# Kernel optimization log

Measured on AMD Instinct MI355X. Metric: run time of the kernel, lower is better.

## Reference

```python
import jax, jax.numpy as jnp
import numpy as np

N = 100000   # nodes
E = 1600000  # edges
G = 64       # graphs
D = 64       # latent_dim
NF = 128     # num_node_feats
EF = 32      # num_edge_feats
NV = 5000    # num_node_val_feats
LV = 3       # max_lv
EPS = 1e-5


def setup_inputs() -> dict:
    key = jax.random.key(0)
    ks = jax.random.split(key, 16)
    s = 0.05
    return {
        "node_feat": jax.random.normal(ks[0], (N, NF), jnp.float32),
        "edge_feat": jax.random.normal(ks[1], (E, EF), jnp.float32),
        "w_n2l_W": jax.random.normal(ks[2], (NF, D), jnp.float32) * s,
        "w_n2l_b": jnp.zeros((D,), jnp.float32),
        "node_val_embedding": jax.random.normal(ks[3], (NV, D), jnp.float32) * s,
        "w_e2l_W": jax.random.normal(ks[4], (LV + 1, EF, D), jnp.float32) * s,
        "w_e2l_b": jnp.zeros((LV + 1, D), jnp.float32),
        "conv_W": jax.random.normal(ks[5], (LV, D, D), jnp.float32) * s,
        "conv_b": jnp.zeros((LV, D), jnp.float32),
        "l2_W": jax.random.normal(ks[6], (LV, D, D), jnp.float32) * s,
        "l2_b": jnp.zeros((LV, D), jnp.float32),
        "msg_g": jnp.ones((LV + 1, D), jnp.float32),
        "msg_b": jnp.zeros((LV + 1, D), jnp.float32),
        "hid_g": jnp.ones((LV, D), jnp.float32),
        "hid_b": jnp.zeros((LV, D), jnp.float32),
        "out_W": jax.random.normal(ks[7], (D, D), jnp.float32) * s,
        "out_b": jnp.zeros((D,), jnp.float32),
        "edge_from": jax.random.randint(ks[8], (E,), 0, N, jnp.int32),
        "edge_to": jax.random.randint(ks[9], (E,), 0, N, jnp.int32),
        "g_idx": jnp.sort(jax.random.randint(ks[10], (N,), 0, G, jnp.int32)),
        "node_val_idx": jax.random.randint(ks[11], (N,), 0, NV, jnp.int32),
    }


def _bn(x, g, b):
    # BatchNorm1d in training mode: biased batch stats
    m = jnp.mean(x, axis=0)
    v = jnp.mean(jnp.square(x - m), axis=0)
    return (x - m) * jax.lax.rsqrt(v + EPS) * g + b


def reference(node_feat, edge_feat, w_n2l_W, w_n2l_b, node_val_embedding,
              w_e2l_W, w_e2l_b, conv_W, conv_b, l2_W, l2_b,
              msg_g, msg_b, hid_g, hid_b, out_W, out_b,
              edge_from, edge_to, g_idx, node_val_idx):
    act = jax.nn.relu
    # input node transform + sparse node-value embedding (one-hot spmm == gather)
    h = node_feat @ w_n2l_W + w_n2l_b + node_val_embedding[node_val_idx]
    # edge->node pool for level 0
    e0 = edge_feat @ w_e2l_W[0] + w_e2l_b[0]
    h = h + jax.ops.segment_sum(e0, edge_to, num_segments=N)
    h = _bn(act(h), msg_g[0], msg_b[0])
    for lv in range(LV):
        # MessagePassing with add-aggr: gather sources, scatter-add to targets, then Linear
        agg = jax.ops.segment_sum(h[edge_from], edge_to, num_segments=N)
        node_linear = agg @ conv_W[lv] + conv_b[lv]
        e = edge_feat @ w_e2l_W[lv + 1] + w_e2l_b[lv + 1]
        merged = act(node_linear + jax.ops.segment_sum(e, edge_to, num_segments=N))
        merged = _bn(merged, hid_g[lv], hid_b[lv])
        h = _bn(act(merged @ l2_W[lv] + l2_b[lv] + h), msg_g[lv + 1], msg_b[lv + 1])
    # readout: gnn_out='last', readout_agg='max', act_last=True, bn=False
    pooled = jax.ops.segment_max(h, g_idx, num_segments=G)
    return act(pooled @ out_W + out_b)
```

## Files before the change

kernel.cpp:

```cpp
#include <hip/hip_runtime.h>
#include <math.h>

#define NN 100000
#define EE 1600000
#define GG 64
#define DD 64
#define NF 128
#define EF 32
#define LVL 3
#define EPSBN 1e-5f
#define NTILES ((NN + 63) / 64)
#define NBKT 391

typedef unsigned short u16;
typedef unsigned int u32;
typedef unsigned long long u64;
typedef short s4v __attribute__((ext_vector_type(4)));
typedef short bf16x8 __attribute__((ext_vector_type(8)));
typedef float f32x4 __attribute__((ext_vector_type(4)));

__device__ __forceinline__ float4 ld4(const float* p) { return *(const float4*)p; }
__device__ __forceinline__ u16 f2b(float f) {
    u32 u = __float_as_uint(f);
    return (u16)((u + 0x7FFFu + ((u >> 16) & 1u)) >> 16);
}
__device__ __forceinline__ u32 pk2(float x, float y) {
    return (u32)f2b(x) | ((u32)f2b(y) << 16);
}
__device__ __forceinline__ float b2f(u16 u) { return __uint_as_float(((u32)u) << 16); }
__device__ __forceinline__ float blo(u32 u) { return __uint_as_float(u << 16); }
__device__ __forceinline__ float bhi(u32 u) { return __uint_as_float(u & 0xFFFF0000u); }

__device__ __forceinline__ float2 bn_pair(const float* __restrict__ slot,
                                          const float* __restrict__ g,
                                          const float* __restrict__ b, int ch) {
    float mean = slot[ch] * (1.0f / NN);
    float var = slot[64 + ch] * (1.0f / NN) - mean * mean;
    float sc = g[ch] * rsqrtf(fmaxf(var, 0.f) + EPSBN);
    return make_float2(sc, b[ch] - mean * sc);
}

__global__ void k1b(const int* __restrict__ to, int* __restrict__ bhist) {
    __shared__ int h[NBKT];
    for (int i = threadIdx.x; i < NBKT; i += 256) h[i] = 0;
    __syncthreads();
    for (int e = blockIdx.x * 256 + threadIdx.x; e < EE; e += 256 * gridDim.x)
        atomicAdd(&h[to[e] >> 8], 1);
    __syncthreads();
    for (int i = threadIdx.x; i < NBKT; i += 256)
        if (h[i]) atomicAdd(&bhist[i], h[i]);
}

__global__ void k1c(const int* __restrict__ bhist, int* __restrict__ bbase,
                    int* __restrict__ gcur) {
    __shared__ int s[512];
    int t = threadIdx.x;
    s[t] = (t < NBKT) ? bhist[t] : 0;
    __syncthreads();
    for (int off = 1; off < 512; off <<= 1) {
        int v = (t >= off) ? s[t - off] : 0;
        __syncthreads();
        s[t] += v;
        __syncthreads();
    }
    if (t < NBKT) {
        int base = t ? s[t - 1] : 0;
        bbase[t] = base;
        gcur[t] = base;
    }
    if (t == NBKT - 1) bbase[NBKT] = s[t];
}

__global__ void k1d(const int* __restrict__ to, const int* __restrict__ from,
                    const float* __restrict__ ef, int* __restrict__ gcur,
                    int* __restrict__ tmpw, uint4* __restrict__ tmp_ef) {
    __shared__ int h[NBKT];
    __shared__ int cur[NBKT];
    for (int i = threadIdx.x; i < NBKT; i += 256) h[i] = 0;
    __syncthreads();
    for (int e = blockIdx.x * 256 + threadIdx.x; e < EE; e += 256 * gridDim.x)
        atomicAdd(&h[to[e] >> 8], 1);
    __syncthreads();
    for (int i = threadIdx.x; i < NBKT; i += 256)
        cur[i] = h[i] ? atomicAdd(&gcur[i], h[i]) : 0;
    __syncthreads();
    for (int e = blockIdx.x * 256 + threadIdx.x; e < EE; e += 256 * gridDim.x) {
        int tt = to[e];
        int b = tt >> 8;
        int pos = atomicAdd(&cur[b], 1);
        tmpw[pos] = from[e] | ((tt & 255) << 17);
        const float4* efp = (const float4*)(ef + (size_t)e * EF);
        uint4* dst = tmp_ef + (size_t)pos * 4;
#pragma unroll
        for (int j = 0; j < 4; j++) {
            float4 a = efp[2 * j], b4 = efp[2 * j + 1];
            dst[j] = make_uint4(pk2(a.x, a.y), pk2(a.z, a.w), pk2(b4.x, b4.y),
                                pk2(b4.z, b4.w));
        }
    }
}

__global__ void kp2(const int* __restrict__ tmpw, const uint4* __restrict__ tmp_ef,
                    const int* __restrict__ bbase, int* __restrict__ row_ptr,
                    int* __restrict__ src_s, int* __restrict__ perm,
                    u16* __restrict__ pooled) {
    __shared__ int s[256];
    __shared__ int cur[256];
    int b = blockIdx.x, t = threadIdx.x;
    int e0 = bbase[b], e1 = bbase[b + 1];
    s[t] = 0;
    __syncthreads();
    for (int e = e0 + t; e < e1; e += 256) atomicAdd(&s[(tmpw[e] >> 17) & 255], 1);
    __syncthreads();
    int v = s[t];
    for (int off = 1; off < 256; off <<= 1) {
        int u = (t >= off) ? s[t - off] : 0;
        __syncthreads();
        s[t] += u;
        __syncthreads();
    }
    int excl = e0 + s[t] - v;
    cur[t] = excl;
    int n = b * 256 + t;
    if (n < NN) row_ptr[n] = excl;
    if (b == NBKT - 1 && t == 0) row_ptr[NN] = e1;
    __syncthreads();
    for (int e = e0 + t; e < e1; e += 256) {
        int w = tmpw[e];
        int pos = atomicAdd(&cur[(w >> 17) & 255], 1);
        src_s[pos] = w & 0x1FFFF;
        perm[pos] = e;
    }
    __threadfence_block();
    __syncthreads();
    if (n < NN) {
        float av[EF];
#pragma unroll
        for (int c = 0; c < EF; c++) av[c] = 0.f;
        for (int i = 0; i < v; i++) {
            int e = perm[excl + i];
            const uint4* p = tmp_ef + (size_t)e * 4;
            uint4 q0 = p[0], q1 = p[1], q2 = p[2], q3 = p[3];
            av[0] += blo(q0.x); av[1] += bhi(q0.x); av[2] += blo(q0.y); av[3] += bhi(q0.y);
            av[4] += blo(q0.z); av[5] += bhi(q0.z); av[6] += blo(q0.w); av[7] += bhi(q0.w);
            av[8] += blo(q1.x); av[9] += bhi(q1.x); av[10] += blo(q1.y); av[11] += bhi(q1.y);
            av[12] += blo(q1.z); av[13] += bhi(q1.z); av[14] += blo(q1.w); av[15] += bhi(q1.w);
            av[16] += blo(q2.x); av[17] += bhi(q2.x); av[18] += blo(q2.y); av[19] += bhi(q2.y);
            av[20] += blo(q2.z); av[21] += bhi(q2.z); av[22] += blo(q2.w); av[23] += bhi(q2.w);
            av[24] += blo(q3.x); av[25] += bhi(q3.x); av[26] += blo(q3.y); av[27] += bhi(q3.y);
            av[28] += blo(q3.z); av[29] += bhi(q3.z); av[30] += blo(q3.w); av[31] += bhi(q3.w);
        }
        u32 orow[16];
#pragma unroll
        for (int j = 0; j < 16; j++) orow[j] = pk2(av[2 * j], av[2 * j + 1]);
        uint4* pr = (uint4*)((u32*)pooled + (size_t)n * 16);
        pr[0] = make_uint4(orow[0], orow[1], orow[2], orow[3]);
        pr[1] = make_uint4(orow[4], orow[5], orow[6], orow[7]);
        pr[2] = make_uint4(orow[8], orow[9], orow[10], orow[11]);
        pr[3] = make_uint4(orow[12], orow[13], orow[14], orow[15]);
    }
}

template <int K1, int K2, bool A1BF, bool AAFF, bool EMB, bool BE, bool RESID>
__global__ __launch_bounds__(256) void kgemm_mfma(
    const void* __restrict__ A1v, const u16* __restrict__ A2,
    const float* __restrict__ W1, const float* __restrict__ W2,
    const float* __restrict__ bias, const float* __restrict__ be,
    const int* __restrict__ row_ptr, const float* __restrict__ emb,
    const int* __restrict__ nvi, const u16* __restrict__ resid,
    const float* __restrict__ rslot, const float* __restrict__ rg,
    const float* __restrict__ rb, const float* __restrict__ aslot,
    const float* __restrict__ ag, const float* __restrict__ ab,
    u16* __restrict__ Xb, float* __restrict__ stats) {
    constexpr int K = K1 + K2;
    constexpr int KP = K + 8;
    __shared__ u16 A_lds[64 * KP];
    __shared__ u16 Wt_lds[64 * KP];
    __shared__ float red[128];
    __shared__ float affl[128];

    const int t = threadIdx.x;
    const int lane = t & 63;
    const int wv = t >> 6;
    const int l15 = lane & 15;
    const int lg = lane >> 4;

    for (int idx = t; idx < K * 16; idx += 256) {
        int k = idx >> 4, c4 = (idx & 15) * 4;
        float4 w4 = (k < K1) ? ld4(W1 + (size_t)k * 64 + c4)
                             : ld4(W2 + (size_t)(k - K1) * 64 + c4);
        Wt_lds[(c4 + 0) * KP + k] = f2b(w4.x);
        Wt_lds[(c4 + 1) * KP + k] = f2b(w4.y);
        Wt_lds[(c4 + 2) * KP + k] = f2b(w4.z);
        Wt_lds[(c4 + 3) * KP + k] = f2b(w4.w);
    }
    if (t < 128) red[t] = 0.f;
    if (AAFF && t < 64) {
        float2 p = bn_pair(aslot, ag, ab, t);
        affl[t] = p.x;
        affl[64 + t] = p.y;
    }

    float bias_c[4], be_c[4], rsc_c[4], rsh_c[4];
#pragma unroll
    for (int n = 0; n < 4; n++) {
        int ch = 16 * n + l15;
        bias_c[n] = bias[ch];
        be_c[n] = BE ? be[ch] : 0.f;
        if (RESID) {
            float2 p = bn_pair(rslot, rg, rb, ch);
            rsc_c[n] = p.x;
            rsh_c[n] = p.y;
        } else {
            rsc_c[n] = 0.f;
            rsh_c[n] = 0.f;
        }
    }

    for (int tile = blockIdx.x; tile < NTILES; tile += gridDim.x) {
        int nb = tile * 64;
        __syncthreads();
        if (A1BF) {
            const u16* A1b = (const u16*)A1v;
            for (int idx = t; idx < 64 * (K1 / 4); idx += 256) {
                int node = idx / (K1 / 4), kq = (idx % (K1 / 4)) * 4;
                int gn = nb + node;
                s4v v = {0, 0, 0, 0};
                if (gn < NN) {
                    v = *(const s4v*)(A1b + (size_t)gn * K1 + kq);
                    if (AAFF) {
#pragma unroll
                        for (int i = 0; i < 4; i++) {
                            float f = b2f((u16)v[i]) * affl[kq + i] + affl[64 + kq + i];
                            v[i] = (short)f2b(f);
                        }
                    }
                }
                *(s4v*)&A_lds[node * KP + kq] = v;
            }
        } else {
            const float* A1f = (const float*)A1v;
            for (int idx = t; idx < 64 * (K1 / 4); idx += 256) {
                int node = idx / (K1 / 4), kq = (idx % (K1 / 4)) * 4;
                int gn = nb + node;
                s4v v = {0, 0, 0, 0};
                if (gn < NN) {
                    float4 a = ld4(A1f + (size_t)gn * K1 + kq);
                    v[0] = (short)f2b(a.x); v[1] = (short)f2b(a.y);
                    v[2] = (short)f2b(a.z); v[3] = (short)f2b(a.w);
                }
                *(s4v*)&A_lds[node * KP + kq] = v;
            }
        }
        if (K2 > 0) {
            for (int idx = t; idx < 64 * (K2 / 4); idx += 256) {
                int node = idx / (K2 / 4), kq = (idx % (K2 / 4)) * 4;
                int gn = nb + node;
                s4v v = {0, 0, 0, 0};
                if (gn < NN) v = *(const s4v*)(A2 + (size_t)gn * K2 + kq);
                *(s4v*)&A_lds[node * KP + K1 + kq] = v;
            }
        }
        __syncthreads();

        f32x4 acc[4];
#pragma unroll
        for (int n = 0; n < 4; n++) acc[n] = (f32x4){0.f, 0.f, 0.f, 0.f};
        const int arow = 16 * wv + l15;
#pragma unroll
        for (int kk = 0; kk < K; kk += 32) {
            s4v alo = *(const s4v*)&A_lds[arow * KP + kk + lg * 4];
            s4v ahi = *(const s4v*)&A_lds[arow * KP + kk + lg * 4 + 16];
            bf16x8 a = __builtin_shufflevector(alo, ahi, 0, 1, 2, 3, 4, 5, 6, 7);
#pragma unroll
            for (int n = 0; n < 4; n++) {
                s4v wlo = *(const s4v*)&Wt_lds[(16 * n + l15) * KP + kk + lg * 4];
                s4v whi = *(const s4v*)&Wt_lds[(16 * n + l15) * KP + kk + lg * 4 + 16];
                bf16x8 b = __builtin_shufflevector(wlo, whi, 0, 1, 2, 3, 4, 5, 6, 7);
                acc[n] = __builtin_amdgcn_mfma_f32_16x16x32_bf16(a, b, acc[n], 0, 0, 0);
            }
        }

        float ss[4] = {0, 0, 0, 0}, sq2[4] = {0, 0, 0, 0};
#pragma unroll
        for (int r = 0; r < 4; r++) {
            int node = nb + 16 * wv + lg * 4 + r;
            if (node < NN) {
                float deg = BE ? (float)(row_ptr[node + 1] - row_ptr[node]) : 0.f;
                int nv = EMB ? nvi[node] : 0;
#pragma unroll
                for (int n = 0; n < 4; n++) {
                    int ch = 16 * n + l15;
                    float v = acc[n][r] + bias_c[n];
                    if (BE) v += deg * be_c[n];
                    if (EMB) v += emb[(size_t)nv * 64 + ch];
                    if (RESID) v += b2f(resid[(size_t)node * 64 + ch]) * rsc_c[n] + rsh_c[n];
                    v = fmaxf(v, 0.f);
                    Xb[(size_t)node * 64 + ch] = f2b(v);
                    ss[n] += v;
                    sq2[n] += v * v;
                }
            }
        }
#pragma unroll
        for (int n = 0; n < 4; n++) {
            float a = ss[n];
            a += __shfl_xor(a, 16);
            a += __shfl_xor(a, 32);
            float b = sq2[n];
            b += __shfl_xor(b, 16);
            b += __shfl_xor(b, 32);
            if (lg == 0) {
                atomicAdd(&red[16 * n + l15], a);
                atomicAdd(&red[64 + 16 * n + l15], b);
            }
        }
    }
    __syncthreads();
    if (t < 128) atomicAdd(&stats[t], red[t]);
}

__global__ void kmsg_bf(const u64* __restrict__ h4, const int* __restrict__ row_ptr,
                        const int* __restrict__ src_s, const float* __restrict__ slot,
                        const float* __restrict__ g, const float* __restrict__ bb,
                        u64* __restrict__ agg) {
    int lane = threadIdx.x & 63;
    int wid = threadIdx.x >> 6;
    int w = lane & 15, sl = lane >> 4;
    float2 p0 = bn_pair(slot, g, bb, 4 * w);
    float2 p1 = bn_pair(slot, g, bb, 4 * w + 1);
    float2 p2 = bn_pair(slot, g, bb, 4 * w + 2);
    float2 p3 = bn_pair(slot, g, bb, 4 * w + 3);
    for (int n = blockIdx.x * 4 + wid; n < NN; n += gridDim.x * 4) {
        int e0 = row_ptr[n], e1 = row_ptr[n + 1];
        float a0 = 0.f, a1 = 0.f, a2 = 0.f, a3 = 0.f;
        int e = e0 + sl;
        for (; e + 12 < e1; e += 16) {
            int s0 = src_s[e], s1 = src_s[e + 4], s2 = src_s[e + 8], s3 = src_s[e + 12];
            u64 v0 = h4[(size_t)s0 * 16 + w];
            u64 v1 = h4[(size_t)s1 * 16 + w];
            u64 v2 = h4[(size_t)s2 * 16 + w];
            u64 v3 = h4[(size_t)s3 * 16 + w];
            u32 l0 = (u32)v0, h0 = (u32)(v0 >> 32);
            u32 l1 = (u32)v1, h1 = (u32)(v1 >> 32);
            u32 l2 = (u32)v2, h2w = (u32)(v2 >> 32);
            u32 l3 = (u32)v3, h3 = (u32)(v3 >> 32);
            a0 += (blo(l0) + blo(l1)) + (blo(l2) + blo(l3));
            a1 += (bhi(l0) + bhi(l1)) + (bhi(l2) + bhi(l3));
            a2 += (blo(h0) + blo(h1)) + (blo(h2w) + blo(h3));
            a3 += (bhi(h0) + bhi(h1)) + (bhi(h2w) + bhi(h3));
        }
        for (; e < e1; e += 4) {
            u64 v = h4[(size_t)src_s[e] * 16 + w];
            u32 l = (u32)v, h = (u32)(v >> 32);
            a0 += blo(l);
            a1 += bhi(l);
            a2 += blo(h);
            a3 += bhi(h);
        }
        a0 += __shfl_xor(a0, 16);
        a0 += __shfl_xor(a0, 32);
        a1 += __shfl_xor(a1, 16);
        a1 += __shfl_xor(a1, 32);
        a2 += __shfl_xor(a2, 16);
        a2 += __shfl_xor(a2, 32);
        a3 += __shfl_xor(a3, 16);
        a3 += __shfl_xor(a3, 32);
        if (sl == 0) {
            float deg = (float)(e1 - e0);
            u32 lo = pk2(p0.x * a0 + deg * p0.y, p1.x * a1 + deg * p1.y);
            u32 hi = pk2(p2.x * a2 + deg * p2.y, p3.x * a3 + deg * p3.y);
            agg[(size_t)n * 16 + w] = (u64)lo | ((u64)hi << 32);
        }
    }
}

__device__ __forceinline__ unsigned fenc(float f) {
    unsigned u = __float_as_uint(f);
    return (u >> 31) ? ~u : (u | 0x80000000u);
}
__device__ __forceinline__ float fdec(unsigned k) {
    return (k >> 31) ? __uint_as_float(k ^ 0x80000000u) : __uint_as_float(~k);
}

__global__ void kinitpk(unsigned* __restrict__ pk) {
    int i = blockIdx.x * blockDim.x + threadIdx.x;
    if (i < GG * DD) pk[i] = 0x007FFFFFu;
}

__global__ void kread(const u16* __restrict__ h2, const int* __restrict__ gidx,
                      const float* __restrict__ slot, const float* __restrict__ g,
                      const float* __restrict__ bb, unsigned* __restrict__ pk) {
    int lane = threadIdx.x & 63;
    int wid = threadIdx.x >> 6;
    float2 p = bn_pair(slot, g, bb, lane);
    float sc = p.x, sh = p.y;
    int gw = blockIdx.x * 4 + wid;
    int nw = gridDim.x * 4;
    int chunk = (NN + nw - 1) / nw;
    int lo = gw * chunk, hi = min(lo + chunk, NN);
    if (lo >= hi) return;
    int cur = gidx[lo];
    float acc = -INFINITY;
    for (int n = lo; n < hi; n++) {
        int gg = gidx[n];
        if (gg != cur) {
            atomicMax(&pk[cur * DD + lane], fenc(acc));
            cur = gg;
            acc = -INFINITY;
        }
        acc = fmaxf(acc, b2f(h2[(size_t)n * 64 + lane]) * sc + sh);
    }
    atomicMax(&pk[cur * DD + lane], fenc(acc));
}

__global__ void kout(const unsigned* __restrict__ pk, const float* __restrict__ W,
                     const float* __restrict__ b, float* __restrict__ out) {
    int t = blockIdx.x * blockDim.x + threadIdx.x;
    int g = t >> 6, d = t & 63;
    float acc = b[d];
    for (int k = 0; k < DD; k++) {
        float p = fdec(pk[g * DD + k]);
        acc += p * W[k * DD + d];
    }
    out[t] = fmaxf(acc, 0.f);
}

extern "C" void kernel_launch(void* const* d_in, const int* in_sizes, int n_in,
                              void* d_out, int out_size, void* d_ws, size_t ws_size,
                              hipStream_t stream) {
    const float* node_feat = (const float*)d_in[0];
    const float* edge_feat = (const float*)d_in[1];
    const float* w_n2l_W = (const float*)d_in[2];
    const float* w_n2l_b = (const float*)d_in[3];
    const float* nve = (const float*)d_in[4];
    const float* w_e2l_W = (const float*)d_in[5];
    const float* w_e2l_b = (const float*)d_in[6];
    const float* conv_W = (const float*)d_in[7];
    const float* conv_b = (const float*)d_in[8];
    const float* l2_W = (const float*)d_in[9];
    const float* l2_b = (const float*)d_in[10];
    const float* msg_g = (const float*)d_in[11];
    const float* msg_b = (const float*)d_in[12];
    const float* hid_g = (const float*)d_in[13];
    const float* hid_b = (const float*)d_in[14];
    const float* out_W = (const float*)d_in[15];
    const float* out_b = (const float*)d_in[16];
    const int* edge_from = (const int*)d_in[17];
    const int* edge_to = (const int*)d_in[18];
    const int* g_idx = (const int*)d_in[19];
    const int* nvi = (const int*)d_in[20];
    float* out = (float*)d_out;

    char* ws = (char*)d_ws;
    size_t off = 0;
    auto alloc = [&](size_t bytes) -> void* {
        void* p = ws + off;
        off += (bytes + 255) / 256 * 256;
        return p;
    };
    int* row_ptr = (int*)alloc((size_t)(NN + 1) * 4);
    int* src_s = (int*)alloc((size_t)EE * 4);
    int* perm = (int*)alloc((size_t)EE * 4);
    int* tmpw = (int*)alloc((size_t)EE * 4);
    uint4* tmp_ef = (uint4*)alloc((size_t)EE * 64);
    u16* pooled_ef = (u16*)alloc((size_t)NN * EF * 2);
    u16* h2a = (u16*)alloc((size_t)NN * DD * 2);
    u16* h2b = (u16*)alloc((size_t)NN * DD * 2);
    u16* agg_bf = (u16*)alloc((size_t)NN * DD * 2);
    u16* mb_bf = (u16*)alloc((size_t)NN * DD * 2);
    float* stats = (float*)alloc(1024 * 4);
    unsigned* pk = (unsigned*)alloc((size_t)GG * DD * 4);
    int* bhist = (int*)alloc((size_t)NBKT * 4);
    int* bbase = (int*)alloc((size_t)(NBKT + 1) * 4);
    int* gcur = (int*)alloc((size_t)NBKT * 4);
    (void)ws_size; (void)n_in; (void)in_sizes; (void)out_size;

    hipMemsetAsync(bhist, 0, (size_t)NBKT * 4, stream);
    hipMemsetAsync(stats, 0, 1024 * 4, stream);
    kinitpk<<<16, 256, 0, stream>>>(pk);

    k1b<<<256, 256, 0, stream>>>(edge_to, bhist);
    k1c<<<1, 512, 0, stream>>>(bhist, bbase, gcur);
    k1d<<<512, 256, 0, stream>>>(edge_to, edge_from, edge_feat, gcur, tmpw, tmp_ef);
    kp2<<<NBKT, 256, 0, stream>>>(tmpw, tmp_ef, bbase, row_ptr, src_s, perm, pooled_ef);

    const int GB = 782;
    const float* S = stats;

    kgemm_mfma<NF, EF, false, false, true, true, false>
        <<<GB, 256, 0, stream>>>(node_feat, pooled_ef, w_n2l_W, w_e2l_W,
                                 w_n2l_b, w_e2l_b, row_ptr, nve, nvi, nullptr,
                                 nullptr, nullptr, nullptr, nullptr, nullptr, nullptr,
                                 h2a, stats + 0 * 128);

    u16* hcur = h2a;
    u16* hnext = h2b;
    for (int lv = 0; lv < LVL; lv++) {
        kmsg_bf<<<4096, 256, 0, stream>>>((const u64*)hcur, row_ptr, src_s,
                                          S + lv * 128, msg_g + lv * 64, msg_b + lv * 64,
                                          (u64*)agg_bf);
        kgemm_mfma<DD, EF, true, false, false, true, false>
            <<<GB, 256, 0, stream>>>(agg_bf, pooled_ef, conv_W + lv * DD * DD,
                                     w_e2l_W + (size_t)(lv + 1) * EF * DD,
                                     conv_b + lv * DD,
                                     w_e2l_b + (size_t)(lv + 1) * DD, row_ptr,
                                     nullptr, nullptr, nullptr, nullptr, nullptr,
                                     nullptr, nullptr, nullptr, nullptr,
                                     mb_bf, stats + (4 + lv) * 128);
        kgemm_mfma<DD, 0, true, true, false, false, true>
            <<<GB, 256, 0, stream>>>(mb_bf, nullptr, l2_W + lv * DD * DD, nullptr,
                                     l2_b + lv * DD, nullptr, row_ptr, nullptr,
                                     nullptr, hcur,
                                     S + lv * 128, msg_g + lv * 64, msg_b + lv * 64,
                                     S + (4 + lv) * 128, hid_g + lv * 64, hid_b + lv * 64,
                                     hnext, stats + (lv + 1) * 128);
        u16* tsw = hcur; hcur = hnext; hnext = tsw;
    }

    kread<<<1024, 256, 0, stream>>>(hcur, g_idx, S + LVL * 128, msg_g + LVL * 64,
                                    msg_b + LVL * 64, pk);
    kout<<<GG, 64, 0, stream>>>(pk, out_W, out_b, out);
}
```

Measured before the change: 626.4 us.

## Pool edge features from sorted edge ids instead of staging bf16 copies

Result: faster. 610.8 us (-2.5%).

```diff
diff --git a/kernel.cpp b/kernel.cpp
--- a/kernel.cpp
+++ b/kernel.cpp
@@ -72,8 +72,7 @@
 }
 
 __global__ void k1d(const int* __restrict__ to, const int* __restrict__ from,
-                    const float* __restrict__ ef, int* __restrict__ gcur,
-                    int* __restrict__ tmpw, uint4* __restrict__ tmp_ef) {
+                    int* __restrict__ gcur, int2* __restrict__ tmp) {
     __shared__ int h[NBKT];
     __shared__ int cur[NBKT];
     for (int i = threadIdx.x; i < NBKT; i += 256) h[i] = 0;
@@ -88,29 +87,20 @@
         int tt = to[e];
         int b = tt >> 8;
         int pos = atomicAdd(&cur[b], 1);
-        tmpw[pos] = from[e] | ((tt & 255) << 17);
-        const float4* efp = (const float4*)(ef + (size_t)e * EF);
-        uint4* dst = tmp_ef + (size_t)pos * 4;
-#pragma unroll
-        for (int j = 0; j < 4; j++) {
-            float4 a = efp[2 * j], b4 = efp[2 * j + 1];
-            dst[j] = make_uint4(pk2(a.x, a.y), pk2(a.z, a.w), pk2(b4.x, b4.y),
-                                pk2(b4.z, b4.w));
-        }
-    }
-}
-
-__global__ void kp2(const int* __restrict__ tmpw, const uint4* __restrict__ tmp_ef,
-                    const int* __restrict__ bbase, int* __restrict__ row_ptr,
-                    int* __restrict__ src_s, int* __restrict__ perm,
-                    u16* __restrict__ pooled) {
+        tmp[pos] = make_int2(from[e] | ((tt & 255) << 17), e);
+    }
+}
+
+__global__ void kp2(const int2* __restrict__ tmp, const int* __restrict__ bbase,
+                    int* __restrict__ row_ptr, int* __restrict__ src_s,
+                    int* __restrict__ eid_s) {
     __shared__ int s[256];
     __shared__ int cur[256];
     int b = blockIdx.x, t = threadIdx.x;
     int e0 = bbase[b], e1 = bbase[b + 1];
     s[t] = 0;
     __syncthreads();
-    for (int e = e0 + t; e < e1; e += 256) atomicAdd(&s[(tmpw[e] >> 17) & 255], 1);
+    for (int e = e0 + t; e < e1; e += 256) atomicAdd(&s[(tmp[e].x >> 17) & 255], 1);
     __syncthreads();
     int v = s[t];
     for (int off = 1; off < 256; off <<= 1) {
@@ -126,38 +116,41 @@
     if (b == NBKT - 1 && t == 0) row_ptr[NN] = e1;
     __syncthreads();
     for (int e = e0 + t; e < e1; e += 256) {
-        int w = tmpw[e];
-        int pos = atomicAdd(&cur[(w >> 17) & 255], 1);
-        src_s[pos] = w & 0x1FFFF;
-        perm[pos] = e;
-    }
-    __threadfence_block();
-    __syncthreads();
-    if (n < NN) {
-        float av[EF];
-#pragma unroll
-        for (int c = 0; c < EF; c++) av[c] = 0.f;
-        for (int i = 0; i < v; i++) {
-            int e = perm[excl + i];
-            const uint4* p = tmp_ef + (size_t)e * 4;
-            uint4 q0 = p[0], q1 = p[1], q2 = p[2], q3 = p[3];
-            av[0] += blo(q0.x); av[1] += bhi(q0.x); av[2] += blo(q0.y); av[3] += bhi(q0.y);
-            av[4] += blo(q0.z); av[5] += bhi(q0.z); av[6] += blo(q0.w); av[7] += bhi(q0.w);
-            av[8] += blo(q1.x); av[9] += bhi(q1.x); av[10] += blo(q1.y); av[11] += bhi(q1.y);
-            av[12] += blo(q1.z); av[13] += bhi(q1.z); av[14] += blo(q1.w); av[15] += bhi(q1.w);
-            av[16] += blo(q2.x); av[17] += bhi(q2.x); av[18] += blo(q2.y); av[19] += bhi(q2.y);
-            av[20] += blo(q2.z); av[21] += bhi(q2.z); av[22] += blo(q2.w); av[23] += bhi(q2.w);
-            av[24] += blo(q3.x); av[25] += bhi(q3.x); av[26] += blo(q3.y); av[27] += bhi(q3.y);
-            av[28] += blo(q3.z); av[29] += bhi(q3.z); av[30] += blo(q3.w); av[31] += bhi(q3.w);
-        }
-        u32 orow[16];
-#pragma unroll
-        for (int j = 0; j < 16; j++) orow[j] = pk2(av[2 * j], av[2 * j + 1]);
-        uint4* pr = (uint4*)((u32*)pooled + (size_t)n * 16);
-        pr[0] = make_uint4(orow[0], orow[1], orow[2], orow[3]);
-        pr[1] = make_uint4(orow[4], orow[5], orow[6], orow[7]);
-        pr[2] = make_uint4(orow[8], orow[9], orow[10], orow[11]);
-        pr[3] = make_uint4(orow[12], orow[13], orow[14], orow[15]);
+        int2 w = tmp[e];
+        int pos = atomicAdd(&cur[(w.x >> 17) & 255], 1);
+        src_s[pos] = w.x & 0x1FFFF;
+        eid_s[pos] = w.y;
+    }
+}
+
+__global__ void kpool(const float* __restrict__ ef, const int* __restrict__ row_ptr,
+                      const int* __restrict__ eid_s, u16* __restrict__ pooled) {
+    int lane = threadIdx.x & 63;
+    int wid = threadIdx.x >> 6;
+    int w = lane & 15, slot = lane >> 4;
+    for (int n = blockIdx.x * 4 + wid; n < NN; n += gridDim.x * 4) {
+        int e0 = row_ptr[n], e1 = row_ptr[n + 1];
+        float ax = 0.f, ay = 0.f;
+        int e = e0 + slot;
+        for (; e + 12 < e1; e += 16) {
+            int i0 = eid_s[e], i1 = eid_s[e + 4], i2 = eid_s[e + 8], i3 = eid_s[e + 12];
+            float2 v0 = *(const float2*)(ef + (size_t)i0 * EF + 2 * w);
+            float2 v1 = *(const float2*)(ef + (size_t)i1 * EF + 2 * w);
+            float2 v2 = *(const float2*)(ef + (size_t)i2 * EF + 2 * w);
+            float2 v3 = *(const float2*)(ef + (size_t)i3 * EF + 2 * w);
+            ax += (v0.x + v1.x) + (v2.x + v3.x);
+            ay += (v0.y + v1.y) + (v2.y + v3.y);
+        }
+        for (; e < e1; e += 4) {
+            float2 v = *(const float2*)(ef + (size_t)eid_s[e] * EF + 2 * w);
+            ax += v.x;
+            ay += v.y;
+        }
+        ax += __shfl_xor(ax, 16);
+        ax += __shfl_xor(ax, 32);
+        ay += __shfl_xor(ay, 16);
+        ay += __shfl_xor(ay, 32);
+        if (slot == 0) *(u32*)&pooled[(size_t)n * EF + 2 * w] = pk2(ax, ay);
     }
 }
 
@@ -388,30 +381,45 @@
     if (i < GG * DD) pk[i] = 0x007FFFFFu;
 }
 
-__global__ void kread(const u16* __restrict__ h2, const int* __restrict__ gidx,
+__global__ void kread(const u64* __restrict__ h4, const int* __restrict__ gidx,
                       const float* __restrict__ slot, const float* __restrict__ g,
                       const float* __restrict__ bb, unsigned* __restrict__ pk) {
     int lane = threadIdx.x & 63;
     int wid = threadIdx.x >> 6;
-    float2 p = bn_pair(slot, g, bb, lane);
-    float sc = p.x, sh = p.y;
+    int w = lane & 15, sl = lane >> 4;
+    float2 p0 = bn_pair(slot, g, bb, 4 * w);
+    float2 p1 = bn_pair(slot, g, bb, 4 * w + 1);
+    float2 p2 = bn_pair(slot, g, bb, 4 * w + 2);
+    float2 p3 = bn_pair(slot, g, bb, 4 * w + 3);
     int gw = blockIdx.x * 4 + wid;
     int nw = gridDim.x * 4;
     int chunk = (NN + nw - 1) / nw;
     int lo = gw * chunk, hi = min(lo + chunk, NN);
-    if (lo >= hi) return;
-    int cur = gidx[lo];
-    float acc = -INFINITY;
-    for (int n = lo; n < hi; n++) {
+    int n = lo + sl;
+    if (n >= hi) return;
+    int cur = gidx[n];
+    float m0 = -INFINITY, m1 = -INFINITY, m2 = -INFINITY, m3 = -INFINITY;
+    for (; n < hi; n += 4) {
         int gg = gidx[n];
         if (gg != cur) {
-            atomicMax(&pk[cur * DD + lane], fenc(acc));
+            atomicMax(&pk[cur * DD + 4 * w + 0], fenc(m0));
+            atomicMax(&pk[cur * DD + 4 * w + 1], fenc(m1));
+            atomicMax(&pk[cur * DD + 4 * w + 2], fenc(m2));
+            atomicMax(&pk[cur * DD + 4 * w + 3], fenc(m3));
             cur = gg;
-            acc = -INFINITY;
-        }
-        acc = fmaxf(acc, b2f(h2[(size_t)n * 64 + lane]) * sc + sh);
-    }
-    atomicMax(&pk[cur * DD + lane], fenc(acc));
+            m0 = m1 = m2 = m3 = -INFINITY;
+        }
+        u64 v = h4[(size_t)n * 16 + w];
+        u32 l = (u32)v, h = (u32)(v >> 32);
+        m0 = fmaxf(m0, blo(l) * p0.x + p0.y);
+        m1 = fmaxf(m1, bhi(l) * p1.x + p1.y);
+        m2 = fmaxf(m2, blo(h) * p2.x + p2.y);
+        m3 = fmaxf(m3, bhi(h) * p3.x + p3.y);
+    }
+    atomicMax(&pk[cur * DD + 4 * w + 0], fenc(m0));
+    atomicMax(&pk[cur * DD + 4 * w + 1], fenc(m1));
+    atomicMax(&pk[cur * DD + 4 * w + 2], fenc(m2));
+    atomicMax(&pk[cur * DD + 4 * w + 3], fenc(m3));
 }
 
 __global__ void kout(const unsigned* __restrict__ pk, const float* __restrict__ W,
@@ -461,9 +469,8 @@
     };
     int* row_ptr = (int*)alloc((size_t)(NN + 1) * 4);
     int* src_s = (int*)alloc((size_t)EE * 4);
-    int* perm = (int*)alloc((size_t)EE * 4);
-    int* tmpw = (int*)alloc((size_t)EE * 4);
-    uint4* tmp_ef = (uint4*)alloc((size_t)EE * 64);
+    int* eid_s = (int*)alloc((size_t)EE * 4);
+    int2* tmp = (int2*)alloc((size_t)EE * 8);
     u16* pooled_ef = (u16*)alloc((size_t)NN * EF * 2);
     u16* h2a = (u16*)alloc((size_t)NN * DD * 2);
     u16* h2b = (u16*)alloc((size_t)NN * DD * 2);
@@ -482,8 +489,9 @@
 
     k1b<<<256, 256, 0, stream>>>(edge_to, bhist);
     k1c<<<1, 512, 0, stream>>>(bhist, bbase, gcur);
-    k1d<<<512, 256, 0, stream>>>(edge_to, edge_from, edge_feat, gcur, tmpw, tmp_ef);
-    kp2<<<NBKT, 256, 0, stream>>>(tmpw, tmp_ef, bbase, row_ptr, src_s, perm, pooled_ef);
+    k1d<<<256, 256, 0, stream>>>(edge_to, edge_from, gcur, tmp);
+    kp2<<<NBKT, 256, 0, stream>>>(tmp, bbase, row_ptr, src_s, eid_s);
+    kpool<<<4096, 256, 0, stream>>>(edge_feat, row_ptr, eid_s, pooled_ef);
 
     const int GB = 782;
     const float* S = stats;
@@ -518,7 +526,7 @@
         u16* tsw = hcur; hcur = hnext; hnext = tsw;
     }
 
-    kread<<<1024, 256, 0, stream>>>(hcur, g_idx, S + LVL * 128, msg_g + LVL * 64,
-                                    msg_b + LVL * 64, pk);
+    kread<<<1024, 256, 0, stream>>>((const u64*)hcur, g_idx, S + LVL * 128,
+                                    msg_g + LVL * 64, msg_b + LVL * 64, pk);
     kout<<<GG, 64, 0, stream>>>(pk, out_W, out_b, out);
 }
```
